# Optimization experiments

Hardware: AMD Instinct MI355X
Metric: run time of the kernel (lower is better)

## Reference

```python
import jax, jax.numpy as jnp
import numpy as np

N_ATOMS = 131072
NUM_GS = 128
HIDDEN = 512
N_MOL = 1024


def setup_inputs() -> dict:
    key = jax.random.key(0)
    ks = jax.random.split(key, 16)
    Gs = jax.random.normal(ks[0], (N_ATOMS, NUM_GS), dtype=jnp.float32)
    types = jax.random.randint(ks[1], (N_ATOMS,), 0, 2, dtype=jnp.int32)
    mol_id = jnp.sort(jax.random.randint(ks[2], (N_ATOMS,), 0, N_MOL, dtype=jnp.int32))

    def dense(k, fi, fo):
        return (jax.random.normal(k, (fi, fo), dtype=jnp.float32) / np.float32(np.sqrt(fi)))

    params = {}
    for i, t in enumerate(("A", "B")):
        base = 3 + i * 3
        params[f"W1_{t}"] = dense(ks[base], NUM_GS, HIDDEN)
        params[f"b1_{t}"] = jnp.zeros((HIDDEN,), jnp.float32)
        params[f"W2_{t}"] = dense(ks[base + 1], HIDDEN, HIDDEN)
        params[f"b2_{t}"] = jnp.zeros((HIDDEN,), jnp.float32)
        params[f"W3_{t}"] = dense(ks[base + 2], HIDDEN, 1)
        params[f"b3_{t}"] = jnp.zeros((1,), jnp.float32)
        params[f"off_{t}"] = jnp.zeros((1,), jnp.float32)
    return {"Gs": Gs, "types": types, "mol_id": mol_id, **params}


def _ann(G, W1, b1, W2, b2, W3, b3, off):
    # Atomic NN: two tanh hidden layers, linear scalar output + trainable offset
    h = jnp.tanh(G @ W1 + b1)
    h = jnp.tanh(h @ W2 + b2)
    return (h @ W3 + b3 + off)[:, 0]  # [N]


def reference(Gs, types, mol_id,
              W1_A, b1_A, W2_A, b2_A, W3_A, b3_A, off_A,
              W1_B, b1_B, W2_B, b2_B, W3_B, b3_B, off_B):
    # Per-type expert MLPs; dense-select is the math-equivalent of
    # dynamic_partition -> per-type ANN -> dynamic_stitch for 2 experts.
    eA = _ann(Gs, W1_A, b1_A, W2_A, b2_A, W3_A, b3_A, off_A)
    eB = _ann(Gs, W1_B, b1_B, W2_B, b2_B, W3_B, b3_B, off_B)
    atom_e = jnp.where(types == 0, eA, eB)  # [N_ATOMS]
    # Ragged per-molecule reduce_sum == segment_sum over sorted mol ids
    mol_e = jax.ops.segment_sum(atom_e, mol_id, num_segments=N_MOL)
    counts = jax.ops.segment_sum(jnp.ones_like(atom_e), mol_id, num_segments=N_MOL)
    energy_per_atom = mol_e / jnp.maximum(counts, 1.0)
    return energy_per_atom[:, None]  # [N_MOL, 1]
```

## Files before the change

### kernel.cpp

```cpp
#include <hip/hip_runtime.h>

typedef _Float16 half8  __attribute__((ext_vector_type(8)));
typedef _Float16 half4v __attribute__((ext_vector_type(4)));
typedef __fp16   fp16x2 __attribute__((ext_vector_type(2)));
typedef float    floatx4 __attribute__((ext_vector_type(4)));

#define N_ATOMS 131072
#define NUM_GS  128
#define HIDDEN  512
#define N_MOL   1024

#define BM      64
#define NB_SIDE (N_ATOMS / BM)
#define NT_TOT  (HIDDEN / 16)
#define SH1_LD  (HIDDEN + 8)
#define SGH_LD  (NUM_GS + 8)

#define WS_CNT_OFF     0
#define WS_MOLSUM_OFF  1024
#define WS_PERM_OFF    9216
#define WS_W1FA_OFF    533504
#define WS_W1FB_OFF    664576
#define WS_W2FA_OFF    795648
#define WS_W2FB_OFF    1319936
#define WS_ZERO_BYTES  5120

__device__ __forceinline__ float fast_tanh(float x) {
    float e = exp2f(x * 2.8853900817779268f);
    float r = __builtin_amdgcn_rcpf(e + 1.0f);
    return fmaf(-2.0f, r, 1.0f);
}

__global__ __launch_bounds__(256)
void prep_kernel(const int* __restrict__ types,
                 const float* __restrict__ W1A, const float* __restrict__ W1B,
                 const float* __restrict__ W2A, const float* __restrict__ W2B,
                 int* __restrict__ cnt, int* __restrict__ perm,
                 _Float16* __restrict__ W1FA, _Float16* __restrict__ W1FB,
                 _Float16* __restrict__ W2FA, _Float16* __restrict__ W2FB) {
    __shared__ float tile[32][65];
    const int p   = blockIdx.x;
    const int tid = threadIdx.x;

    if (p < 512) {
        __shared__ int sCA[4];
        __shared__ int sBaseA, sBaseB;
        const int i    = p * 256 + tid;
        const int lane = tid & 63;
        const int w    = tid >> 6;
        const bool isA = (types[i] == 0);
        unsigned long long mask = __ballot(isA);
        unsigned long long lt   = ((unsigned long long)1 << lane) - 1;
        int rA = __popcll(mask & lt);
        if (lane == 0) sCA[w] = __popcll(mask);
        __syncthreads();
        if (tid == 0) {
            int tot = sCA[0] + sCA[1] + sCA[2] + sCA[3];
            sBaseA = atomicAdd(&cnt[0], tot);
            sBaseB = atomicAdd(&cnt[1], 256 - tot);
        }
        __syncthreads();
        int preA = 0;
        #pragma unroll
        for (int k = 0; k < 4; ++k) preA += (k < w) ? sCA[k] : 0;
        int preB = w * 64 - preA;
        int rB   = lane - rA;
        if (isA) perm[sBaseA + preA + rA] = i;
        else     perm[N_ATOMS - 1 - (sBaseB + preB + rB)] = i;
        return;
    }

    const float* src; _Float16* dst; int pb;
    if (p < 544)      { src = W1A; dst = W1FA; pb = p - 512; }
    else if (p < 576) { src = W1B; dst = W1FB; pb = p - 544; }
    else if (p < 704) { src = W2A; dst = W2FA; pb = p - 576; }
    else              { src = W2B; dst = W2FB; pb = p - 704; }
    const int bx = pb & 7;
    const int by = pb >> 3;
    const int n0 = bx * 64, k0 = by * 32;
    #pragma unroll
    for (int i = 0; i < 8; ++i) {
        int idx = tid + i * 256;
        int r = idx >> 6, c = idx & 63;
        tile[r][c] = src[(size_t)(k0 + r) * HIDDEN + n0 + c];
    }
    __syncthreads();
    const int nt_l = tid >> 6, lane = tid & 63;
    const int l15 = lane & 15, q = lane >> 4;
    half8 v;
    #pragma unroll
    for (int j = 0; j < 8; ++j)
        v[j] = (_Float16)tile[q * 8 + j][nt_l * 16 + l15];
    const int ntile = bx * 4 + nt_l;
    *(half8*)(dst + (((size_t)by * NT_TOT + ntile) * 64 + lane) * 8) = v;
}

__global__ __launch_bounds__(512, 4)
void mlp_kernel(const float* __restrict__ Gs,
                const int*   __restrict__ mol_id,
                const _Float16* __restrict__ W1FA, const _Float16* __restrict__ W2FA,
                const float* __restrict__ b1A, const float* __restrict__ b2A,
                const float* __restrict__ W3A, const float* __restrict__ b3A,
                const float* __restrict__ offA,
                const _Float16* __restrict__ W1FB, const _Float16* __restrict__ W2FB,
                const float* __restrict__ b1B, const float* __restrict__ b2B,
                const float* __restrict__ W3B, const float* __restrict__ b3B,
                const float* __restrict__ offB,
                const int* __restrict__ cnt, const int* __restrict__ perm,
                float* __restrict__ mol_sum) {
    __shared__ __align__(16) _Float16 sBuf[BM * SH1_LD];
    __shared__ int   sOrig[BM];
    __shared__ float sPart[8][BM];

    _Float16 (*sH1)[SH1_LD] = (_Float16(*)[SH1_LD])sBuf;
    _Float16 (*sGh)[SGH_LD] = (_Float16(*)[SGH_LD])sBuf;

    const int b     = blockIdx.x;
    const int nA    = cnt[0];
    const int sideB = (b >= NB_SIDE) ? 1 : 0;
    const int r0    = (sideB ? b - NB_SIDE : b) * BM;
    const int nSide = sideB ? (N_ATOMS - nA) : nA;
    if (r0 >= nSide) return;

    const _Float16 *W1F, *W2F;
    const float *b1, *b2, *W3;
    float b3off;
    if (!sideB) { W1F = W1FA; W2F = W2FA; b1 = b1A; b2 = b2A; W3 = W3A; b3off = b3A[0] + offA[0]; }
    else        { W1F = W1FB; W2F = W2FB; b1 = b1B; b2 = b2B; W3 = W3B; b3off = b3B[0] + offB[0]; }

    const int tid = threadIdx.x;
    if (tid < BM) {
        int r = r0 + tid;
        int orig = -1;
        if (r < nSide) orig = sideB ? perm[N_ATOMS - 1 - r] : perm[r];
        sOrig[tid] = orig;
    }
    __syncthreads();

    #pragma unroll
    for (int i = 0; i < 4; ++i) {
        int idx = tid + 512 * i;
        int row = idx >> 5;
        int c4  = idx & 31;
        int orig = sOrig[row];
        float4 v = make_float4(0.f, 0.f, 0.f, 0.f);
        if (orig >= 0) v = ((const float4*)(Gs + (size_t)orig * NUM_GS))[c4];
        union { half4v h4; fp16x2 h2[2]; } hu;
        hu.h2[0] = __builtin_amdgcn_cvt_pkrtz(v.x, v.y);
        hu.h2[1] = __builtin_amdgcn_cvt_pkrtz(v.z, v.w);
        *(half4v*)&sGh[row][c4 * 4] = hu.h4;
    }
    __syncthreads();

    const int lane = tid & 63;
    const int wid  = tid >> 6;
    const int l15  = lane & 15;
    const int quad = lane >> 4;

    floatx4 acc[4][4];
    #pragma unroll
    for (int mt = 0; mt < 4; ++mt)
        #pragma unroll
        for (int nt = 0; nt < 4; ++nt) acc[mt][nt] = (floatx4){0.f, 0.f, 0.f, 0.f};

    #pragma unroll 2
    for (int ks = 0; ks < NUM_GS / 32; ++ks) {
        half8 a[4];
        #pragma unroll
        for (int mt = 0; mt < 4; ++mt)
            a[mt] = *(const half8*)&sGh[mt * 16 + l15][ks * 32 + quad * 8];
        #pragma unroll
        for (int nt = 0; nt < 4; ++nt) {
            int ntile = wid * 4 + nt;
            half8 bf = *(const half8*)(W1F + (((size_t)ks * NT_TOT + ntile) * 64 + lane) * 8);
            #pragma unroll
            for (int mt = 0; mt < 4; ++mt)
                acc[mt][nt] = __builtin_amdgcn_mfma_f32_16x16x32_f16(a[mt], bf, acc[mt][nt], 0, 0, 0);
        }
    }
    __syncthreads();

    #pragma unroll
    for (int nt = 0; nt < 4; ++nt) {
        int col = wid * 64 + nt * 16 + l15;
        float b1v = b1[col];
        #pragma unroll
        for (int mt = 0; mt < 4; ++mt)
            #pragma unroll
            for (int r = 0; r < 4; ++r)
                sH1[mt * 16 + quad * 4 + r][col] = (_Float16)fast_tanh(acc[mt][nt][r] + b1v);
    }
    __syncthreads();

    #pragma unroll
    for (int mt = 0; mt < 4; ++mt)
        #pragma unroll
        for (int nt = 0; nt < 4; ++nt) acc[mt][nt] = (floatx4){0.f, 0.f, 0.f, 0.f};

    #pragma unroll 2
    for (int ks = 0; ks < HIDDEN / 32; ++ks) {
        half8 a[4];
        #pragma unroll
        for (int mt = 0; mt < 4; ++mt)
            a[mt] = *(const half8*)&sH1[mt * 16 + l15][ks * 32 + quad * 8];
        #pragma unroll
        for (int nt = 0; nt < 4; ++nt) {
            int ntile = wid * 4 + nt;
            half8 bf = *(const half8*)(W2F + (((size_t)ks * NT_TOT + ntile) * 64 + lane) * 8);
            #pragma unroll
            for (int mt = 0; mt < 4; ++mt)
                acc[mt][nt] = __builtin_amdgcn_mfma_f32_16x16x32_f16(a[mt], bf, acc[mt][nt], 0, 0, 0);
        }
    }

    float p[4][4];
    #pragma unroll
    for (int mt = 0; mt < 4; ++mt)
        #pragma unroll
        for (int r = 0; r < 4; ++r) p[mt][r] = 0.f;

    #pragma unroll
    for (int nt = 0; nt < 4; ++nt) {
        int col = wid * 64 + nt * 16 + l15;
        float b2v = b2[col];
        float w3v = W3[col];
        #pragma unroll
        for (int mt = 0; mt < 4; ++mt)
            #pragma unroll
            for (int r = 0; r < 4; ++r) {
                float t = fast_tanh(acc[mt][nt][r] + b2v);
                p[mt][r] = fmaf(t, w3v, p[mt][r]);
            }
    }
    #pragma unroll
    for (int mt = 0; mt < 4; ++mt)
        #pragma unroll
        for (int r = 0; r < 4; ++r) {
            float v = p[mt][r];
            v += __shfl_xor(v, 1, 64);
            v += __shfl_xor(v, 2, 64);
            v += __shfl_xor(v, 4, 64);
            v += __shfl_xor(v, 8, 64);
            p[mt][r] = v;
        }
    if (l15 == 0) {
        #pragma unroll
        for (int mt = 0; mt < 4; ++mt)
            #pragma unroll
            for (int r = 0; r < 4; ++r)
                sPart[wid][mt * 16 + quad * 4 + r] = p[mt][r];
    }
    __syncthreads();
    if (tid < BM) {
        int orig = sOrig[tid];
        if (orig >= 0) {
            float e = b3off;
            #pragma unroll
            for (int w = 0; w < 8; ++w) e += sPart[w][tid];
            atomicAdd(&mol_sum[mol_id[orig]], e);
        }
    }
}

__global__ void finalize_kernel(const float* __restrict__ mol_sum,
                                const int* __restrict__ mol_id,
                                float* __restrict__ out) {
    int m = blockIdx.x * blockDim.x + threadIdx.x;
    if (m >= N_MOL) return;
    int lo0 = 0, hi0 = N_ATOMS;
    while (lo0 < hi0) { int mid = (lo0 + hi0) >> 1; if (mol_id[mid] < m) lo0 = mid + 1; else hi0 = mid; }
    int lo1 = lo0, hi1 = N_ATOMS;
    while (lo1 < hi1) { int mid = (lo1 + hi1) >> 1; if (mol_id[mid] < m + 1) lo1 = mid + 1; else hi1 = mid; }
    float c = (float)(lo1 - lo0);
    out[m] = mol_sum[m] / fmaxf(c, 1.0f);
}

extern "C" void kernel_launch(void* const* d_in, const int* in_sizes, int n_in,
                              void* d_out, int out_size, void* d_ws, size_t ws_size,
                              hipStream_t stream) {
    const float* Gs     = (const float*)d_in[0];
    const int*   types  = (const int*)d_in[1];
    const int*   mol_id = (const int*)d_in[2];
    const float* W1A = (const float*)d_in[3];
    const float* b1A = (const float*)d_in[4];
    const float* W2A = (const float*)d_in[5];
    const float* b2A = (const float*)d_in[6];
    const float* W3A = (const float*)d_in[7];
    const float* b3A = (const float*)d_in[8];
    const float* oA  = (const float*)d_in[9];
    const float* W1B = (const float*)d_in[10];
    const float* b1B = (const float*)d_in[11];
    const float* W2B = (const float*)d_in[12];
    const float* b2B = (const float*)d_in[13];
    const float* W3B = (const float*)d_in[14];
    const float* b3B = (const float*)d_in[15];
    const float* oB  = (const float*)d_in[16];

    char* ws = (char*)d_ws;
    int*      cnt     = (int*)(ws + WS_CNT_OFF);
    float*    mol_sum = (float*)(ws + WS_MOLSUM_OFF);
    int*      perm    = (int*)(ws + WS_PERM_OFF);
    _Float16* W1FA    = (_Float16*)(ws + WS_W1FA_OFF);
    _Float16* W1FB    = (_Float16*)(ws + WS_W1FB_OFF);
    _Float16* W2FA    = (_Float16*)(ws + WS_W2FA_OFF);
    _Float16* W2FB    = (_Float16*)(ws + WS_W2FB_OFF);
    float* out = (float*)d_out;

    hipMemsetAsync(d_ws, 0, WS_ZERO_BYTES, stream);
    prep_kernel<<<832, 256, 0, stream>>>(types, W1A, W1B, W2A, W2B,
                                         cnt, perm,
                                         W1FA, W1FB, W2FA, W2FB);
    mlp_kernel<<<2 * NB_SIDE, 512, 0, stream>>>(
        Gs, mol_id,
        W1FA, W2FA, b1A, b2A, W3A, b3A, oA,
        W1FB, W2FB, b1B, b2B, W3B, b3B, oB,
        cnt, perm, mol_sum);
    finalize_kernel<<<(N_MOL + 255) / 256, 256, 0, stream>>>(mol_sum, mol_id, out);
}
```

Baseline: 282.9 us.

## Switch MLP GEMMs to 32x32x16 MFMA with transposed operand layout

Replaces the 16x16x32 MFMA tiling with 32x32x16 MFMA. Weights are now the A operand and atoms the B operand, so each lane's accumulator holds contiguous hidden columns for a single atom. The weight pre-swizzle kernel is rewritten to match. Biases are preloaded into the accumulators, and layer-1 outputs are packed into vector fp16 stores. The final W3 reduction becomes mostly in-register and needs only one cross-half shuffle. The intent is fewer MFMA issues, fewer LDS operand loads per FLOP, and a cheaper epilogue, at the cost of a different register footprint.

Measured after the change: 280.6 us. About the same (-0.8%).

```diff
diff --git a/kernel.cpp b/kernel.cpp
--- a/kernel.cpp
+++ b/kernel.cpp
@@ -3,7 +3,7 @@
 typedef _Float16 half8  __attribute__((ext_vector_type(8)));
 typedef _Float16 half4v __attribute__((ext_vector_type(4)));
 typedef __fp16   fp16x2 __attribute__((ext_vector_type(2)));
-typedef float    floatx4 __attribute__((ext_vector_type(4)));
+typedef float    floatx16 __attribute__((ext_vector_type(16)));
 
 #define N_ATOMS 131072
 #define NUM_GS  128
@@ -12,7 +12,7 @@
 
 #define BM      64
 #define NB_SIDE (N_ATOMS / BM)
-#define NT_TOT  (HIDDEN / 16)
+#define NT32    (HIDDEN / 32)
 #define SH1_LD  (HIDDEN + 8)
 #define SGH_LD  (NUM_GS + 8)
 
@@ -85,14 +85,16 @@
         tile[r][c] = src[(size_t)(k0 + r) * HIDDEN + n0 + c];
     }
     __syncthreads();
-    const int nt_l = tid >> 6, lane = tid & 63;
-    const int l15 = lane & 15, q = lane >> 4;
+    const int w = tid >> 6, lane = tid & 63;
+    const int l5 = lane & 31, h = lane >> 5;
+    const int ks_l = w >> 1, nt_l = w & 1;
     half8 v;
     #pragma unroll
     for (int j = 0; j < 8; ++j)
-        v[j] = (_Float16)tile[q * 8 + j][nt_l * 16 + l15];
-    const int ntile = bx * 4 + nt_l;
-    *(half8*)(dst + (((size_t)by * NT_TOT + ntile) * 64 + lane) * 8) = v;
+        v[j] = (_Float16)tile[ks_l * 16 + h * 8 + j][nt_l * 32 + l5];
+    const int ksg = by * 2 + ks_l;
+    const int ntg = bx * 2 + nt_l;
+    *(half8*)(dst + (((size_t)ksg * NT32 + ntg) * 64 + lane) * 8) = v;
 }
 
 __global__ __launch_bounds__(512, 4)
@@ -154,101 +156,107 @@
 
     const int lane = tid & 63;
     const int wid  = tid >> 6;
-    const int l15  = lane & 15;
-    const int quad = lane >> 4;
-
-    floatx4 acc[4][4];
-    #pragma unroll
-    for (int mt = 0; mt < 4; ++mt)
-        #pragma unroll
-        for (int nt = 0; nt < 4; ++nt) acc[mt][nt] = (floatx4){0.f, 0.f, 0.f, 0.f};
+    const int l5   = lane & 31;
+    const int h    = lane >> 5;
+
+    floatx16 acc[2][2];
+
+    #pragma unroll
+    for (int nt = 0; nt < 2; ++nt)
+        #pragma unroll
+        for (int g = 0; g < 4; ++g) {
+            const float4 bv = *(const float4*)&b1[wid * 64 + nt * 32 + g * 8 + h * 4];
+            acc[0][nt][g * 4 + 0] = bv.x; acc[1][nt][g * 4 + 0] = bv.x;
+            acc[0][nt][g * 4 + 1] = bv.y; acc[1][nt][g * 4 + 1] = bv.y;
+            acc[0][nt][g * 4 + 2] = bv.z; acc[1][nt][g * 4 + 2] = bv.z;
+            acc[0][nt][g * 4 + 3] = bv.w; acc[1][nt][g * 4 + 3] = bv.w;
+        }
 
     #pragma unroll 2
-    for (int ks = 0; ks < NUM_GS / 32; ++ks) {
-        half8 a[4];
-        #pragma unroll
-        for (int mt = 0; mt < 4; ++mt)
-            a[mt] = *(const half8*)&sGh[mt * 16 + l15][ks * 32 + quad * 8];
-        #pragma unroll
-        for (int nt = 0; nt < 4; ++nt) {
-            int ntile = wid * 4 + nt;
-            half8 bf = *(const half8*)(W1F + (((size_t)ks * NT_TOT + ntile) * 64 + lane) * 8);
-            #pragma unroll
-            for (int mt = 0; mt < 4; ++mt)
-                acc[mt][nt] = __builtin_amdgcn_mfma_f32_16x16x32_f16(a[mt], bf, acc[mt][nt], 0, 0, 0);
-        }
-    }
-    __syncthreads();
-
-    #pragma unroll
-    for (int nt = 0; nt < 4; ++nt) {
-        int col = wid * 64 + nt * 16 + l15;
-        float b1v = b1[col];
-        #pragma unroll
-        for (int mt = 0; mt < 4; ++mt)
-            #pragma unroll
-            for (int r = 0; r < 4; ++r)
-                sH1[mt * 16 + quad * 4 + r][col] = (_Float16)fast_tanh(acc[mt][nt][r] + b1v);
-    }
-    __syncthreads();
-
-    #pragma unroll
-    for (int mt = 0; mt < 4; ++mt)
-        #pragma unroll
-        for (int nt = 0; nt < 4; ++nt) acc[mt][nt] = (floatx4){0.f, 0.f, 0.f, 0.f};
+    for (int ks = 0; ks < NUM_GS / 16; ++ks) {
+        half8 gb[2];
+        #pragma unroll
+        for (int mt = 0; mt < 2; ++mt)
+            gb[mt] = *(const half8*)&sGh[mt * 32 + l5][ks * 16 + h * 8];
+        #pragma unroll
+        for (int nt = 0; nt < 2; ++nt) {
+            const int ntile = wid * 2 + nt;
+            half8 wa = *(const half8*)(W1F + (((size_t)ks * NT32 + ntile) * 64 + lane) * 8);
+            #pragma unroll
+            for (int mt = 0; mt < 2; ++mt)
+                acc[mt][nt] = __builtin_amdgcn_mfma_f32_32x32x16_f16(wa, gb[mt], acc[mt][nt], 0, 0, 0);
+        }
+    }
+    __syncthreads();
+
+    #pragma unroll
+    for (int mt = 0; mt < 2; ++mt)
+        #pragma unroll
+        for (int nt = 0; nt < 2; ++nt)
+            #pragma unroll
+            for (int g = 0; g < 4; ++g) {
+                float t0 = fast_tanh(acc[mt][nt][g * 4 + 0]);
+                float t1 = fast_tanh(acc[mt][nt][g * 4 + 1]);
+                float t2 = fast_tanh(acc[mt][nt][g * 4 + 2]);
+                float t3 = fast_tanh(acc[mt][nt][g * 4 + 3]);
+                union { half4v h4; fp16x2 h2[2]; } hu;
+                hu.h2[0] = __builtin_amdgcn_cvt_pkrtz(t0, t1);
+                hu.h2[1] = __builtin_amdgcn_cvt_pkrtz(t2, t3);
+                *(half4v*)&sH1[mt * 32 + l5][wid * 64 + nt * 32 + g * 8 + h * 4] = hu.h4;
+            }
+    __syncthreads();
+
+    #pragma unroll
+    for (int nt = 0; nt < 2; ++nt)
+        #pragma unroll
+        for (int g = 0; g < 4; ++g) {
+            const float4 bv = *(const float4*)&b2[wid * 64 + nt * 32 + g * 8 + h * 4];
+            acc[0][nt][g * 4 + 0] = bv.x; acc[1][nt][g * 4 + 0] = bv.x;
+            acc[0][nt][g * 4 + 1] = bv.y; acc[1][nt][g * 4 + 1] = bv.y;
+            acc[0][nt][g * 4 + 2] = bv.z; acc[1][nt][g * 4 + 2] = bv.z;
+            acc[0][nt][g * 4 + 3] = bv.w; acc[1][nt][g * 4 + 3] = bv.w;
+        }
 
     #pragma unroll 2
-    for (int ks = 0; ks < HIDDEN / 32; ++ks) {
-        half8 a[4];
-        #pragma unroll
-        for (int mt = 0; mt < 4; ++mt)
-            a[mt] = *(const half8*)&sH1[mt * 16 + l15][ks * 32 + quad * 8];
-        #pragma unroll
-        for (int nt = 0; nt < 4; ++nt) {
-            int ntile = wid * 4 + nt;
-            half8 bf = *(const half8*)(W2F + (((size_t)ks * NT_TOT + ntile) * 64 + lane) * 8);
-            #pragma unroll
-            for (int mt = 0; mt < 4; ++mt)
-                acc[mt][nt] = __builtin_amdgcn_mfma_f32_16x16x32_f16(a[mt], bf, acc[mt][nt], 0, 0, 0);
-        }
-    }
-
-    float p[4][4];
-    #pragma unroll
-    for (int mt = 0; mt < 4; ++mt)
-        #pragma unroll
-        for (int r = 0; r < 4; ++r) p[mt][r] = 0.f;
-
-    #pragma unroll
-    for (int nt = 0; nt < 4; ++nt) {
-        int col = wid * 64 + nt * 16 + l15;
-        float b2v = b2[col];
-        float w3v = W3[col];
-        #pragma unroll
-        for (int mt = 0; mt < 4; ++mt)
-            #pragma unroll
-            for (int r = 0; r < 4; ++r) {
-                float t = fast_tanh(acc[mt][nt][r] + b2v);
-                p[mt][r] = fmaf(t, w3v, p[mt][r]);
+    for (int ks = 0; ks < HIDDEN / 16; ++ks) {
+        half8 hb[2];
+        #pragma unroll
+        for (int mt = 0; mt < 2; ++mt)
+            hb[mt] = *(const half8*)&sH1[mt * 32 + l5][ks * 16 + h * 8];
+        #pragma unroll
+        for (int nt = 0; nt < 2; ++nt) {
+            const int ntile = wid * 2 + nt;
+            half8 wa = *(const half8*)(W2F + (((size_t)ks * NT32 + ntile) * 64 + lane) * 8);
+            #pragma unroll
+            for (int mt = 0; mt < 2; ++mt)
+                acc[mt][nt] = __builtin_amdgcn_mfma_f32_32x32x16_f16(wa, hb[mt], acc[mt][nt], 0, 0, 0);
+        }
+    }
+
+    float4 w3v[2][4];
+    #pragma unroll
+    for (int nt = 0; nt < 2; ++nt)
+        #pragma unroll
+        for (int g = 0; g < 4; ++g)
+            w3v[nt][g] = *(const float4*)&W3[wid * 64 + nt * 32 + g * 8 + h * 4];
+
+    float p[2] = {0.f, 0.f};
+    #pragma unroll
+    for (int mt = 0; mt < 2; ++mt)
+        #pragma unroll
+        for (int nt = 0; nt < 2; ++nt)
+            #pragma unroll
+            for (int g = 0; g < 4; ++g) {
+                p[mt] = fmaf(fast_tanh(acc[mt][nt][g * 4 + 0]), w3v[nt][g].x, p[mt]);
+                p[mt] = fmaf(fast_tanh(acc[mt][nt][g * 4 + 1]), w3v[nt][g].y, p[mt]);
+                p[mt] = fmaf(fast_tanh(acc[mt][nt][g * 4 + 2]), w3v[nt][g].z, p[mt]);
+                p[mt] = fmaf(fast_tanh(acc[mt][nt][g * 4 + 3]), w3v[nt][g].w, p[mt]);
             }
-    }
-    #pragma unroll
-    for (int mt = 0; mt < 4; ++mt)
-        #pragma unroll
-        for (int r = 0; r < 4; ++r) {
-            float v = p[mt][r];
-            v += __shfl_xor(v, 1, 64);
-            v += __shfl_xor(v, 2, 64);
-            v += __shfl_xor(v, 4, 64);
-            v += __shfl_xor(v, 8, 64);
-            p[mt][r] = v;
-        }
-    if (l15 == 0) {
-        #pragma unroll
-        for (int mt = 0; mt < 4; ++mt)
-            #pragma unroll
-            for (int r = 0; r < 4; ++r)
-                sPart[wid][mt * 16 + quad * 4 + r] = p[mt][r];
+    #pragma unroll
+    for (int mt = 0; mt < 2; ++mt) {
+        float v = p[mt];
+        v += __shfl_xor(v, 32, 64);
+        if (lane < 32) sPart[wid][mt * 32 + lane] = v;
     }
     __syncthreads();
     if (tid < BM) {
```

## Swap MFMA operands so accumulators are transposed, enabling vectorized epilogues

Applied to the files above, without the earlier changes.

Swaps the A and B operands of the MFMA so each lane holds 4 consecutive hidden columns for one atom row instead of 4 rows for one column. The biases are folded into the accumulator init via float4 loads. The layer-1 activations are packed and stored as half4 vectors into shared memory. The final W3 dot product needs only a 2-step cross-quad shuffle reduction instead of 4 steps per element, which cuts scalar LDS stores, shuffles and epilogue ALU work. It also fully unrolls the first GEMM loop, which could raise register pressure.

Result: no change. 281.3 us, median of 3 (-0.6%).

```diff
diff --git a/kernel.cpp b/kernel.cpp
--- a/kernel.cpp
+++ b/kernel.cpp
@@ -158,97 +158,92 @@
     const int quad = lane >> 4;
 
     floatx4 acc[4][4];
-    #pragma unroll
-    for (int mt = 0; mt < 4; ++mt)
-        #pragma unroll
-        for (int nt = 0; nt < 4; ++nt) acc[mt][nt] = (floatx4){0.f, 0.f, 0.f, 0.f};
-
-    #pragma unroll 2
+
+    #pragma unroll
+    for (int nt = 0; nt < 4; ++nt) {
+        const float4 bv = *(const float4*)&b1[wid * 64 + nt * 16 + quad * 4];
+        #pragma unroll
+        for (int mt = 0; mt < 4; ++mt)
+            acc[mt][nt] = (floatx4){bv.x, bv.y, bv.z, bv.w};
+    }
+
+    #pragma unroll
     for (int ks = 0; ks < NUM_GS / 32; ++ks) {
-        half8 a[4];
+        half8 gb[4];
         #pragma unroll
         for (int mt = 0; mt < 4; ++mt)
-            a[mt] = *(const half8*)&sGh[mt * 16 + l15][ks * 32 + quad * 8];
+            gb[mt] = *(const half8*)&sGh[mt * 16 + l15][ks * 32 + quad * 8];
         #pragma unroll
         for (int nt = 0; nt < 4; ++nt) {
             int ntile = wid * 4 + nt;
-            half8 bf = *(const half8*)(W1F + (((size_t)ks * NT_TOT + ntile) * 64 + lane) * 8);
+            half8 wa = *(const half8*)(W1F + (((size_t)ks * NT_TOT + ntile) * 64 + lane) * 8);
             #pragma unroll
             for (int mt = 0; mt < 4; ++mt)
-                acc[mt][nt] = __builtin_amdgcn_mfma_f32_16x16x32_f16(a[mt], bf, acc[mt][nt], 0, 0, 0);
-        }
-    }
+                acc[mt][nt] = __builtin_amdgcn_mfma_f32_16x16x32_f16(wa, gb[mt], acc[mt][nt], 0, 0, 0);
+        }
+    }
+    __syncthreads();
+
+    #pragma unroll
+    for (int mt = 0; mt < 4; ++mt)
+        #pragma unroll
+        for (int nt = 0; nt < 4; ++nt) {
+            float t0 = fast_tanh(acc[mt][nt][0]);
+            float t1 = fast_tanh(acc[mt][nt][1]);
+            float t2 = fast_tanh(acc[mt][nt][2]);
+            float t3 = fast_tanh(acc[mt][nt][3]);
+            union { half4v h4; fp16x2 h2[2]; } hu;
+            hu.h2[0] = __builtin_amdgcn_cvt_pkrtz(t0, t1);
+            hu.h2[1] = __builtin_amdgcn_cvt_pkrtz(t2, t3);
+            *(half4v*)&sH1[mt * 16 + l15][wid * 64 + nt * 16 + quad * 4] = hu.h4;
+        }
     __syncthreads();
 
     #pragma unroll
     for (int nt = 0; nt < 4; ++nt) {
-        int col = wid * 64 + nt * 16 + l15;
-        float b1v = b1[col];
+        const float4 bv = *(const float4*)&b2[wid * 64 + nt * 16 + quad * 4];
         #pragma unroll
         for (int mt = 0; mt < 4; ++mt)
-            #pragma unroll
-            for (int r = 0; r < 4; ++r)
-                sH1[mt * 16 + quad * 4 + r][col] = (_Float16)fast_tanh(acc[mt][nt][r] + b1v);
-    }
-    __syncthreads();
-
-    #pragma unroll
-    for (int mt = 0; mt < 4; ++mt)
-        #pragma unroll
-        for (int nt = 0; nt < 4; ++nt) acc[mt][nt] = (floatx4){0.f, 0.f, 0.f, 0.f};
+            acc[mt][nt] = (floatx4){bv.x, bv.y, bv.z, bv.w};
+    }
 
     #pragma unroll 2
     for (int ks = 0; ks < HIDDEN / 32; ++ks) {
-        half8 a[4];
+        half8 hb[4];
         #pragma unroll
         for (int mt = 0; mt < 4; ++mt)
-            a[mt] = *(const half8*)&sH1[mt * 16 + l15][ks * 32 + quad * 8];
+            hb[mt] = *(const half8*)&sH1[mt * 16 + l15][ks * 32 + quad * 8];
         #pragma unroll
         for (int nt = 0; nt < 4; ++nt) {
             int ntile = wid * 4 + nt;
-            half8 bf = *(const half8*)(W2F + (((size_t)ks * NT_TOT + ntile) * 64 + lane) * 8);
+            half8 wa = *(const half8*)(W2F + (((size_t)ks * NT_TOT + ntile) * 64 + lane) * 8);
             #pragma unroll
             for (int mt = 0; mt < 4; ++mt)
-                acc[mt][nt] = __builtin_amdgcn_mfma_f32_16x16x32_f16(a[mt], bf, acc[mt][nt], 0, 0, 0);
-        }
-    }
-
-    float p[4][4];
+                acc[mt][nt] = __builtin_amdgcn_mfma_f32_16x16x32_f16(wa, hb[mt], acc[mt][nt], 0, 0, 0);
+        }
+    }
+
+    float4 w3v[4];
+    #pragma unroll
+    for (int nt = 0; nt < 4; ++nt)
+        w3v[nt] = *(const float4*)&W3[wid * 64 + nt * 16 + quad * 4];
+
+    float p[4] = {0.f, 0.f, 0.f, 0.f};
     #pragma unroll
     for (int mt = 0; mt < 4; ++mt)
         #pragma unroll
-        for (int r = 0; r < 4; ++r) p[mt][r] = 0.f;
-
-    #pragma unroll
-    for (int nt = 0; nt < 4; ++nt) {
-        int col = wid * 64 + nt * 16 + l15;
-        float b2v = b2[col];
-        float w3v = W3[col];
-        #pragma unroll
-        for (int mt = 0; mt < 4; ++mt)
-            #pragma unroll
-            for (int r = 0; r < 4; ++r) {
-                float t = fast_tanh(acc[mt][nt][r] + b2v);
-                p[mt][r] = fmaf(t, w3v, p[mt][r]);
-            }
-    }
-    #pragma unroll
-    for (int mt = 0; mt < 4; ++mt)
-        #pragma unroll
-        for (int r = 0; r < 4; ++r) {
-            float v = p[mt][r];
-            v += __shfl_xor(v, 1, 64);
-            v += __shfl_xor(v, 2, 64);
-            v += __shfl_xor(v, 4, 64);
-            v += __shfl_xor(v, 8, 64);
-            p[mt][r] = v;
-        }
-    if (l15 == 0) {
-        #pragma unroll
-        for (int mt = 0; mt < 4; ++mt)
-            #pragma unroll
-            for (int r = 0; r < 4; ++r)
-                sPart[wid][mt * 16 + quad * 4 + r] = p[mt][r];
+        for (int nt = 0; nt < 4; ++nt) {
+            p[mt] = fmaf(fast_tanh(acc[mt][nt][0]), w3v[nt].x, p[mt]);
+            p[mt] = fmaf(fast_tanh(acc[mt][nt][1]), w3v[nt].y, p[mt]);
+            p[mt] = fmaf(fast_tanh(acc[mt][nt][2]), w3v[nt].z, p[mt]);
+            p[mt] = fmaf(fast_tanh(acc[mt][nt][3]), w3v[nt].w, p[mt]);
+        }
+    #pragma unroll
+    for (int mt = 0; mt < 4; ++mt) {
+        float v = p[mt];
+        v += __shfl_xor(v, 16, 64);
+        v += __shfl_xor(v, 32, 64);
+        if (lane < 16) sPart[wid][mt * 16 + lane] = v;
     }
     __syncthreads();
     if (tid < BM) {
```
